# Performance work log

Hardware: AMD Instinct MI355X
Metric: run time of the kernel (lower is better)

Reference implementation:

```python
import jax, jax.numpy as jnp
import numpy as np

ROUTING_ITERS = 3
OUT_CAPS = 64
BETA_V = 1.0
BETA_A = 1.0
EPS = 1e-09


def l2_normalize(x, axis=-1, eps=1e-12):
    # matches tf.nn.l2_normalize: x / sqrt(max(sum(x^2), eps))
    sq = jnp.sum(jnp.square(x), axis=axis, keepdims=True)
    return x * jax.lax.rsqrt(jnp.maximum(sq, eps))


def setup_inputs() -> dict:
    key = jax.random.key(0)
    k1, k2 = jax.random.split(key)
    B, I, O, P = 32, 2048, OUT_CAPS, 16
    votes = jax.random.normal(k1, (B, I, O, P), dtype=jnp.float32)
    activations_in = jax.random.uniform(k2, (B, I), dtype=jnp.float32)
    return {"votes": votes, "activations_in": activations_in}


def reference(votes, activations_in):
    # votes: [B, I, O, P]; activations_in: [B, I]
    B, I, O, P = votes.shape
    A_h = jnp.full((B, O), 1.0 / O, dtype=votes.dtype)          # [B, O]
    Mu_h = l2_normalize(jnp.mean(votes, axis=1), axis=-1)        # [B, O, P]

    votes_norm = l2_normalize(votes, axis=-1)                    # [B, I, O, P]
    a_in = activations_in[:, :, None]                            # [B, I, 1]

    for _ in range(ROUTING_ITERS):
        # agreement cost
        dot = jnp.einsum('biop,bop->bio', votes_norm, Mu_h)      # [B, I, O]
        cost_v = (1.0 - jnp.square(dot)) * BETA_V
        cost_a = jnp.abs(a_in - A_h[:, None, :]) * BETA_A        # [B, I, O]
        log_posterior = -(cost_v + cost_a) + jnp.log(A_h + EPS)[:, None, :]
        R = jax.nn.softmax(log_posterior, axis=2)                # [B, I, O]

        # activation update
        R_sum = jnp.sum(R * a_in, axis=1)                        # [B, O]
        A_h = R_sum / (jnp.sum(R_sum, axis=1, keepdims=True) + EPS)
        A_h = jnp.clip(A_h, EPS, 1.0 - EPS)

        # pose update (weighted mean of votes)
        num = jnp.einsum('bio,biop->bop', R, votes)              # [B, O, P]
        den = jnp.sum(R, axis=1)[:, :, None] + EPS               # [B, O, 1]
        Mu_h = l2_normalize(num / den, axis=-1)

    return Mu_h, A_h
```

## Files before the change

kernel.cpp:

```cpp
#include <hip/hip_runtime.h>
#include <math.h>

#define NB 32
#define NI 2048
#define NO 64
#define NP 16
#define EPSF 1e-9f

__device__ __forceinline__ float wave_max64(float v) {
#pragma unroll
    for (int off = 32; off > 0; off >>= 1) v = fmaxf(v, __shfl_xor(v, off));
    return v;
}
__device__ __forceinline__ float wave_sum64(float v) {
#pragma unroll
    for (int off = 32; off > 0; off >>= 1) v += __shfl_xor(v, off);
    return v;
}

__global__ __launch_bounds__(256) void mean_accum_kernel(
        const float* __restrict__ votes, float* __restrict__ sum_part) {
    const int b    = blockIdx.y;
    const int i0   = blockIdx.x * 64;
    const int wave = threadIdx.x >> 6;
    const int lane = threadIdx.x & 63;

    float s[NP];
#pragma unroll
    for (int p = 0; p < NP; ++p) s[p] = 0.f;

    for (int i = i0 + wave; i < i0 + 64; i += 4) {
        const float4* vp = reinterpret_cast<const float4*>(
            votes + (((size_t)b * NI + i) * NO + lane) * NP);
        float4 v0 = vp[0], v1 = vp[1], v2 = vp[2], v3 = vp[3];
        s[0] += v0.x;  s[1] += v0.y;  s[2] += v0.z;  s[3] += v0.w;
        s[4] += v1.x;  s[5] += v1.y;  s[6] += v1.z;  s[7] += v1.w;
        s[8] += v2.x;  s[9] += v2.y;  s[10] += v2.z; s[11] += v2.w;
        s[12] += v3.x; s[13] += v3.y; s[14] += v3.z; s[15] += v3.w;
    }

    __shared__ float red[4][NO * NP];
#pragma unroll
    for (int p = 0; p < NP; ++p) red[wave][lane * NP + p] = s[p];
    __syncthreads();
    for (int e = threadIdx.x; e < NO * NP; e += 256) {
        float v = red[0][e] + red[1][e] + red[2][e] + red[3][e];
        atomicAdd(&sum_part[(size_t)b * NO * NP + e], v);
    }
}

__global__ void mean_final_kernel(const float* __restrict__ sum_part,
                                  float* __restrict__ Mu, float* __restrict__ A) {
    const int b = blockIdx.x;
    const int o = threadIdx.x;
    const float inv_I = 1.0f / (float)NI;
    float m[NP];
    float ssq = 0.f;
#pragma unroll
    for (int p = 0; p < NP; ++p) {
        m[p] = sum_part[((size_t)b * NO + o) * NP + p] * inv_I;
        ssq += m[p] * m[p];
    }
    float inv = rsqrtf(fmaxf(ssq, 1e-12f));
#pragma unroll
    for (int p = 0; p < NP; ++p)
        Mu[((size_t)b * NO + o) * NP + p] = m[p] * inv;
    A[b * NO + o] = 1.0f / (float)NO;
}

__global__ __launch_bounds__(256) void iter_accum_kernel(
        const float* __restrict__ votes, const float* __restrict__ act,
        const float* __restrict__ Mu, const float* __restrict__ A,
        float* __restrict__ num_part, float* __restrict__ den_part,
        float* __restrict__ rsum_part) {
    const int b    = blockIdx.y;
    const int i0   = blockIdx.x * 64;
    const int wave = threadIdx.x >> 6;
    const int lane = threadIdx.x & 63;

    float mu[NP];
    {
        const float4* mp = reinterpret_cast<const float4*>(
            Mu + ((size_t)b * NO + lane) * NP);
        float4 m0 = mp[0], m1 = mp[1], m2 = mp[2], m3 = mp[3];
        mu[0] = m0.x;  mu[1] = m0.y;  mu[2] = m0.z;  mu[3] = m0.w;
        mu[4] = m1.x;  mu[5] = m1.y;  mu[6] = m1.z;  mu[7] = m1.w;
        mu[8] = m2.x;  mu[9] = m2.y;  mu[10] = m2.z; mu[11] = m2.w;
        mu[12] = m3.x; mu[13] = m3.y; mu[14] = m3.z; mu[15] = m3.w;
    }
    const float Ao   = A[b * NO + lane];
    const float logA = logf(Ao + EPSF);

    float num[NP];
#pragma unroll
    for (int p = 0; p < NP; ++p) num[p] = 0.f;
    float den = 0.f, rs = 0.f;

    for (int i = i0 + wave; i < i0 + 64; i += 4) {
        const float4* vp = reinterpret_cast<const float4*>(
            votes + (((size_t)b * NI + i) * NO + lane) * NP);
        float4 v0 = vp[0], v1 = vp[1], v2 = vp[2], v3 = vp[3];

        float ssq = v0.x * v0.x + v0.y * v0.y + v0.z * v0.z + v0.w * v0.w
                  + v1.x * v1.x + v1.y * v1.y + v1.z * v1.z + v1.w * v1.w
                  + v2.x * v2.x + v2.y * v2.y + v2.z * v2.z + v2.w * v2.w
                  + v3.x * v3.x + v3.y * v3.y + v3.z * v3.z + v3.w * v3.w;
        float dt  = v0.x * mu[0]  + v0.y * mu[1]  + v0.z * mu[2]  + v0.w * mu[3]
                  + v1.x * mu[4]  + v1.y * mu[5]  + v1.z * mu[6]  + v1.w * mu[7]
                  + v2.x * mu[8]  + v2.y * mu[9]  + v2.z * mu[10] + v2.w * mu[11]
                  + v3.x * mu[12] + v3.y * mu[13] + v3.z * mu[14] + v3.w * mu[15];

        float dn = dt * rsqrtf(fmaxf(ssq, 1e-12f));
        float cv = 1.0f - dn * dn;
        float a  = act[b * NI + i];
        float lp = logA - cv - fabsf(a - Ao);

        float mx = wave_max64(lp);
        float e  = __expf(lp - mx);
        float R  = e / wave_sum64(e);

        rs  += R * a;
        den += R;
        num[0]  += R * v0.x; num[1]  += R * v0.y; num[2]  += R * v0.z; num[3]  += R * v0.w;
        num[4]  += R * v1.x; num[5]  += R * v1.y; num[6]  += R * v1.z; num[7]  += R * v1.w;
        num[8]  += R * v2.x; num[9]  += R * v2.y; num[10] += R * v2.z; num[11] += R * v2.w;
        num[12] += R * v3.x; num[13] += R * v3.y; num[14] += R * v3.z; num[15] += R * v3.w;
    }

    __shared__ float red[4][NO * 18];
    float* myred = &red[wave][lane * 18];
#pragma unroll
    for (int p = 0; p < NP; ++p) myred[p] = num[p];
    myred[16] = den;
    myred[17] = rs;
    __syncthreads();
    for (int e = threadIdx.x; e < NO * 18; e += 256) {
        float v = red[0][e] + red[1][e] + red[2][e] + red[3][e];
        int o = e / 18;
        int k = e - o * 18;
        if (k < NP)        atomicAdd(&num_part[((size_t)b * NO + o) * NP + k], v);
        else if (k == 16)  atomicAdd(&den_part[b * NO + o], v);
        else               atomicAdd(&rsum_part[b * NO + o], v);
    }
}

__global__ void finalize_kernel(const float* __restrict__ num_part,
                                const float* __restrict__ den_part,
                                const float* __restrict__ rsum_part,
                                float* __restrict__ Mu_out,
                                float* __restrict__ A_out) {
    const int b = blockIdx.x;
    const int o = threadIdx.x;
    float rsv = rsum_part[b * NO + o];
    float tot = wave_sum64(rsv);
    float Anew = rsv / (tot + EPSF);
    Anew = fminf(fmaxf(Anew, EPSF), 1.0f - EPSF);
    A_out[b * NO + o] = Anew;

    float inv_dn = 1.0f / (den_part[b * NO + o] + EPSF);
    float m[NP];
    float ssq = 0.f;
#pragma unroll
    for (int p = 0; p < NP; ++p) {
        m[p] = num_part[((size_t)b * NO + o) * NP + p] * inv_dn;
        ssq += m[p] * m[p];
    }
    float inv = rsqrtf(fmaxf(ssq, 1e-12f));
#pragma unroll
    for (int p = 0; p < NP; ++p)
        Mu_out[((size_t)b * NO + o) * NP + p] = m[p] * inv;
}

extern "C" void kernel_launch(void* const* d_in, const int* in_sizes, int n_in,
                              void* d_out, int out_size, void* d_ws, size_t ws_size,
                              hipStream_t stream) {
    const float* votes = (const float*)d_in[0];
    const float* act   = (const float*)d_in[1];

    float* Mu_out = (float*)d_out;
    float* A_out  = (float*)d_out + NB * NO * NP;

    float* ws        = (float*)d_ws;
    float* num_part  = ws;
    float* den_part  = ws + 32768;
    float* rsum_part = ws + 34816;
    float* Mu        = ws + 36864;
    float* A         = ws + 69632;

    dim3 grid(NI / 64, NB);
    dim3 blk(256);

    hipMemsetAsync(num_part, 0, (size_t)NB * NO * NP * sizeof(float), stream);
    mean_accum_kernel<<<grid, blk, 0, stream>>>(votes, num_part);
    mean_final_kernel<<<NB, NO, 0, stream>>>(num_part, Mu, A);

    for (int it = 0; it < 3; ++it) {
        hipMemsetAsync(num_part, 0, (size_t)(NB * NO * NP + 2 * NB * NO) * sizeof(float), stream);
        iter_accum_kernel<<<grid, blk, 0, stream>>>(votes, act, Mu, A,
                                                    num_part, den_part, rsum_part);
        float* mo = (it == 2) ? Mu_out : Mu;
        float* ao = (it == 2) ? A_out  : A;
        finalize_kernel<<<NB, NO, 0, stream>>>(num_part, den_part, rsum_part, mo, ao);
    }
}
```

Before: 503.7 us.

## Replace atomic reductions with per-block partials and use DPP wave sums

Each block now writes its partial sums to its own workspace slice instead of doing global atomicAdd. The finalize kernels sum the 32 partials per batch, which also lets the memset launches go away. The softmax drops its max-subtraction and uses a DPP-based wave sum with fast rcp/rsq/log intrinsics, which cuts shuffle and division cost. Skipping the max-subtraction is safe only because the log-posterior is bounded, and the fast intrinsics slightly change precision.

```diff
diff --git a/kernel.cpp b/kernel.cpp
--- a/kernel.cpp
+++ b/kernel.cpp
@@ -5,23 +5,35 @@
 #define NI 2048
 #define NO 64
 #define NP 16
+#define NBLK 32
 #define EPSF 1e-9f
 
-__device__ __forceinline__ float wave_max64(float v) {
-#pragma unroll
-    for (int off = 32; off > 0; off >>= 1) v = fmaxf(v, __shfl_xor(v, off));
-    return v;
-}
-__device__ __forceinline__ float wave_sum64(float v) {
+__device__ __forceinline__ float wave_sum64_shfl(float v) {
 #pragma unroll
     for (int off = 32; off > 0; off >>= 1) v += __shfl_xor(v, off);
     return v;
 }
 
+__device__ __forceinline__ float wave_sum64_dpp(float v) {
+    v += __int_as_float(__builtin_amdgcn_update_dpp(
+        0, __float_as_int(v), 0x111, 0xf, 0xf, false));
+    v += __int_as_float(__builtin_amdgcn_update_dpp(
+        0, __float_as_int(v), 0x112, 0xf, 0xf, false));
+    v += __int_as_float(__builtin_amdgcn_update_dpp(
+        0, __float_as_int(v), 0x114, 0xf, 0xf, false));
+    v += __int_as_float(__builtin_amdgcn_update_dpp(
+        0, __float_as_int(v), 0x118, 0xf, 0xf, false));
+    v += __int_as_float(__builtin_amdgcn_update_dpp(
+        0, __float_as_int(v), 0x142, 0xa, 0xf, false));
+    v += __int_as_float(__builtin_amdgcn_update_dpp(
+        0, __float_as_int(v), 0x143, 0xc, 0xf, false));
+    return __int_as_float(__builtin_amdgcn_readlane(__float_as_int(v), 63));
+}
+
 __global__ __launch_bounds__(256) void mean_accum_kernel(
-        const float* __restrict__ votes, float* __restrict__ sum_part) {
+        const float* __restrict__ votes, float* __restrict__ pm) {
     const int b    = blockIdx.y;
-    const int i0   = blockIdx.x * 64;
+    const int bx   = blockIdx.x;
     const int wave = threadIdx.x >> 6;
     const int lane = threadIdx.x & 63;
 
@@ -29,9 +41,12 @@
 #pragma unroll
     for (int p = 0; p < NP; ++p) s[p] = 0.f;
 
-    for (int i = i0 + wave; i < i0 + 64; i += 4) {
-        const float4* vp = reinterpret_cast<const float4*>(
-            votes + (((size_t)b * NI + i) * NO + lane) * NP);
+    const float* vbase =
+        votes + (((size_t)b * NI + bx * 64 + wave) * NO + lane) * NP;
+#pragma unroll 2
+    for (int k = 0; k < 16; ++k) {
+        const float4* vp =
+            reinterpret_cast<const float4*>(vbase + (size_t)k * 4 * NO * NP);
         float4 v0 = vp[0], v1 = vp[1], v2 = vp[2], v3 = vp[3];
         s[0] += v0.x;  s[1] += v0.y;  s[2] += v0.z;  s[3] += v0.w;
         s[4] += v1.x;  s[5] += v1.y;  s[6] += v1.z;  s[7] += v1.w;
@@ -43,24 +58,30 @@
 #pragma unroll
     for (int p = 0; p < NP; ++p) red[wave][lane * NP + p] = s[p];
     __syncthreads();
-    for (int e = threadIdx.x; e < NO * NP; e += 256) {
-        float v = red[0][e] + red[1][e] + red[2][e] + red[3][e];
-        atomicAdd(&sum_part[(size_t)b * NO * NP + e], v);
-    }
-}
-
-__global__ void mean_final_kernel(const float* __restrict__ sum_part,
+    float* dst = pm + (size_t)(b * NBLK + bx) * (NO * NP);
+    for (int e = threadIdx.x; e < NO * NP; e += 256)
+        dst[e] = red[0][e] + red[1][e] + red[2][e] + red[3][e];
+}
+
+__global__ void mean_final_kernel(const float* __restrict__ pm,
                                   float* __restrict__ Mu, float* __restrict__ A) {
     const int b = blockIdx.x;
     const int o = threadIdx.x;
-    const float inv_I = 1.0f / (float)NI;
     float m[NP];
+#pragma unroll
+    for (int p = 0; p < NP; ++p) m[p] = 0.f;
+    for (int bx = 0; bx < NBLK; ++bx) {
+        const float4* q = reinterpret_cast<const float4*>(
+            pm + (size_t)(b * NBLK + bx) * (NO * NP) + o * NP);
+        float4 q0 = q[0], q1 = q[1], q2 = q[2], q3 = q[3];
+        m[0] += q0.x;  m[1] += q0.y;  m[2] += q0.z;  m[3] += q0.w;
+        m[4] += q1.x;  m[5] += q1.y;  m[6] += q1.z;  m[7] += q1.w;
+        m[8] += q2.x;  m[9] += q2.y;  m[10] += q2.z; m[11] += q2.w;
+        m[12] += q3.x; m[13] += q3.y; m[14] += q3.z; m[15] += q3.w;
+    }
     float ssq = 0.f;
 #pragma unroll
-    for (int p = 0; p < NP; ++p) {
-        m[p] = sum_part[((size_t)b * NO + o) * NP + p] * inv_I;
-        ssq += m[p] * m[p];
-    }
+    for (int p = 0; p < NP; ++p) { m[p] *= (1.0f / NI); ssq += m[p] * m[p]; }
     float inv = rsqrtf(fmaxf(ssq, 1e-12f));
 #pragma unroll
     for (int p = 0; p < NP; ++p)
@@ -71,10 +92,9 @@
 __global__ __launch_bounds__(256) void iter_accum_kernel(
         const float* __restrict__ votes, const float* __restrict__ act,
         const float* __restrict__ Mu, const float* __restrict__ A,
-        float* __restrict__ num_part, float* __restrict__ den_part,
-        float* __restrict__ rsum_part) {
+        float* __restrict__ ppn, float* __restrict__ ppd) {
     const int b    = blockIdx.y;
-    const int i0   = blockIdx.x * 64;
+    const int bx   = blockIdx.x;
     const int wave = threadIdx.x >> 6;
     const int lane = threadIdx.x & 63;
 
@@ -89,16 +109,21 @@
         mu[12] = m3.x; mu[13] = m3.y; mu[14] = m3.z; mu[15] = m3.w;
     }
     const float Ao   = A[b * NO + lane];
-    const float logA = logf(Ao + EPSF);
+    const float logA = __logf(Ao + EPSF);
 
     float num[NP];
 #pragma unroll
     for (int p = 0; p < NP; ++p) num[p] = 0.f;
     float den = 0.f, rs = 0.f;
 
-    for (int i = i0 + wave; i < i0 + 64; i += 4) {
-        const float4* vp = reinterpret_cast<const float4*>(
-            votes + (((size_t)b * NI + i) * NO + lane) * NP);
+    const float* vbase =
+        votes + (((size_t)b * NI + bx * 64 + wave) * NO + lane) * NP;
+    const float* abase = act + b * NI + bx * 64 + wave;
+
+#pragma unroll 2
+    for (int k = 0; k < 16; ++k) {
+        const float4* vp =
+            reinterpret_cast<const float4*>(vbase + (size_t)k * 4 * NO * NP);
         float4 v0 = vp[0], v1 = vp[1], v2 = vp[2], v3 = vp[3];
 
         float ssq = v0.x * v0.x + v0.y * v0.y + v0.z * v0.z + v0.w * v0.w
@@ -110,14 +135,11 @@
                   + v2.x * mu[8]  + v2.y * mu[9]  + v2.z * mu[10] + v2.w * mu[11]
                   + v3.x * mu[12] + v3.y * mu[13] + v3.z * mu[14] + v3.w * mu[15];
 
-        float dn = dt * rsqrtf(fmaxf(ssq, 1e-12f));
-        float cv = 1.0f - dn * dn;
-        float a  = act[b * NI + i];
-        float lp = logA - cv - fabsf(a - Ao);
-
-        float mx = wave_max64(lp);
-        float e  = __expf(lp - mx);
-        float R  = e / wave_sum64(e);
+        float dn = dt * __builtin_amdgcn_rsqf(fmaxf(ssq, 1e-12f));
+        float a  = abase[4 * k];
+        float lp = logA - (1.0f - dn * dn) - fabsf(a - Ao);
+        float e  = __expf(lp);
+        float R  = e * __builtin_amdgcn_rcpf(wave_sum64_dpp(e));
 
         rs  += R * a;
         den += R;
@@ -134,41 +156,59 @@
     myred[16] = den;
     myred[17] = rs;
     __syncthreads();
-    for (int e = threadIdx.x; e < NO * 18; e += 256) {
-        float v = red[0][e] + red[1][e] + red[2][e] + red[3][e];
-        int o = e / 18;
-        int k = e - o * 18;
-        if (k < NP)        atomicAdd(&num_part[((size_t)b * NO + o) * NP + k], v);
-        else if (k == 16)  atomicAdd(&den_part[b * NO + o], v);
-        else               atomicAdd(&rsum_part[b * NO + o], v);
-    }
-}
-
-__global__ void finalize_kernel(const float* __restrict__ num_part,
-                                const float* __restrict__ den_part,
-                                const float* __restrict__ rsum_part,
+    {
+        float* dn_ = ppn + (size_t)(b * NBLK + bx) * (NO * NP);
+        for (int e = threadIdx.x; e < NO * NP; e += 256) {
+            int o = e >> 4, p = e & 15;
+            dn_[e] = red[0][o * 18 + p] + red[1][o * 18 + p]
+                   + red[2][o * 18 + p] + red[3][o * 18 + p];
+        }
+        float* dd_ = ppd + (size_t)(b * NBLK + bx) * (NO * 2);
+        for (int e = threadIdx.x; e < NO * 2; e += 256) {
+            int o = e >> 1, k = 16 + (e & 1);
+            dd_[e] = red[0][o * 18 + k] + red[1][o * 18 + k]
+                   + red[2][o * 18 + k] + red[3][o * 18 + k];
+        }
+    }
+}
+
+__global__ void finalize_kernel(const float* __restrict__ ppn,
+                                const float* __restrict__ ppd,
                                 float* __restrict__ Mu_out,
                                 float* __restrict__ A_out) {
     const int b = blockIdx.x;
     const int o = threadIdx.x;
-    float rsv = rsum_part[b * NO + o];
-    float tot = wave_sum64(rsv);
-    float Anew = rsv / (tot + EPSF);
+    float num[NP];
+#pragma unroll
+    for (int p = 0; p < NP; ++p) num[p] = 0.f;
+    float den = 0.f, rs = 0.f;
+    for (int bx = 0; bx < NBLK; ++bx) {
+        const float4* q = reinterpret_cast<const float4*>(
+            ppn + (size_t)(b * NBLK + bx) * (NO * NP) + o * NP);
+        float4 q0 = q[0], q1 = q[1], q2 = q[2], q3 = q[3];
+        num[0] += q0.x;  num[1] += q0.y;  num[2] += q0.z;  num[3] += q0.w;
+        num[4] += q1.x;  num[5] += q1.y;  num[6] += q1.z;  num[7] += q1.w;
+        num[8] += q2.x;  num[9] += q2.y;  num[10] += q2.z; num[11] += q2.w;
+        num[12] += q3.x; num[13] += q3.y; num[14] += q3.z; num[15] += q3.w;
+        const float2* d = reinterpret_cast<const float2*>(
+            ppd + (size_t)(b * NBLK + bx) * (NO * 2) + o * 2);
+        float2 dv = d[0];
+        den += dv.x;
+        rs  += dv.y;
+    }
+    float tot = wave_sum64_shfl(rs);
+    float Anew = rs / (tot + EPSF);
     Anew = fminf(fmaxf(Anew, EPSF), 1.0f - EPSF);
     A_out[b * NO + o] = Anew;
 
-    float inv_dn = 1.0f / (den_part[b * NO + o] + EPSF);
-    float m[NP];
+    float inv_dn = 1.0f / (den + EPSF);
     float ssq = 0.f;
 #pragma unroll
-    for (int p = 0; p < NP; ++p) {
-        m[p] = num_part[((size_t)b * NO + o) * NP + p] * inv_dn;
-        ssq += m[p] * m[p];
-    }
+    for (int p = 0; p < NP; ++p) { num[p] *= inv_dn; ssq += num[p] * num[p]; }
     float inv = rsqrtf(fmaxf(ssq, 1e-12f));
 #pragma unroll
     for (int p = 0; p < NP; ++p)
-        Mu_out[((size_t)b * NO + o) * NP + p] = m[p] * inv;
+        Mu_out[((size_t)b * NO + o) * NP + p] = num[p] * inv;
 }
 
 extern "C" void kernel_launch(void* const* d_in, const int* in_sizes, int n_in,
@@ -180,26 +220,22 @@
     float* Mu_out = (float*)d_out;
     float* A_out  = (float*)d_out + NB * NO * NP;
 
-    float* ws        = (float*)d_ws;
-    float* num_part  = ws;
-    float* den_part  = ws + 32768;
-    float* rsum_part = ws + 34816;
-    float* Mu        = ws + 36864;
-    float* A         = ws + 69632;
-
-    dim3 grid(NI / 64, NB);
+    float* ws  = (float*)d_ws;
+    float* ppn = ws;
+    float* ppd = ws + NB * NBLK * 1024;
+    float* Mu  = ppd + NB * NBLK * 128;
+    float* A   = Mu + NB * NO * NP;
+
+    dim3 grid(NBLK, NB);
     dim3 blk(256);
 
-    hipMemsetAsync(num_part, 0, (size_t)NB * NO * NP * sizeof(float), stream);
-    mean_accum_kernel<<<grid, blk, 0, stream>>>(votes, num_part);
-    mean_final_kernel<<<NB, NO, 0, stream>>>(num_part, Mu, A);
+    mean_accum_kernel<<<grid, blk, 0, stream>>>(votes, ppn);
+    mean_final_kernel<<<NB, NO, 0, stream>>>(ppn, Mu, A);
 
     for (int it = 0; it < 3; ++it) {
-        hipMemsetAsync(num_part, 0, (size_t)(NB * NO * NP + 2 * NB * NO) * sizeof(float), stream);
-        iter_accum_kernel<<<grid, blk, 0, stream>>>(votes, act, Mu, A,
-                                                    num_part, den_part, rsum_part);
+        iter_accum_kernel<<<grid, blk, 0, stream>>>(votes, act, Mu, A, ppn, ppd);
         float* mo = (it == 2) ? Mu_out : Mu;
         float* ao = (it == 2) ? A_out  : A;
-        finalize_kernel<<<NB, NO, 0, stream>>>(num_part, den_part, rsum_part, mo, ao);
-    }
-}
+        finalize_kernel<<<NB, NO, 0, stream>>>(ppn, ppd, mo, ao);
+    }
+}
```

New measurement: 512.8 us. No clear change (+1.8%).
